# Optimization experiments

Hardware: AMD Instinct MI355X
Metric: run time of the kernel (lower is better)

The kernel has to match this reference:

```python
import jax, jax.numpy as jnp
import numpy as np

B, T, N, E = 8, 16, 2048, 32768
F_IN, C, EDGE_DIM = 32, 32, 1


def setup_inputs() -> dict:
    key = jax.random.key(0)
    ks = jax.random.split(key, 12)
    s = 1.0 / np.sqrt(C)
    x = jax.random.normal(ks[0], (B, T, N, F_IN), jnp.float32)
    edge_index = jax.random.randint(ks[1], (2, E), 0, N)
    edge_attr = jax.random.normal(ks[2], (E, EDGE_DIM), jnp.float32)
    Wl = jax.random.normal(ks[3], (F_IN, C), jnp.float32) * s
    bl = jnp.zeros((C,), jnp.float32)
    Wr = jax.random.normal(ks[4], (F_IN, C), jnp.float32) * s
    br = jnp.zeros((C,), jnp.float32)
    We = jax.random.normal(ks[5], (EDGE_DIM, C), jnp.float32) * s
    att = jax.random.normal(ks[6], (C,), jnp.float32) * s
    out_bias = jnp.zeros((C,), jnp.float32)
    w_ih = jax.random.normal(ks[7], (3 * C, C), jnp.float32) * s
    w_hh = jax.random.normal(ks[8], (3 * C, C), jnp.float32) * s
    b_ih = jnp.zeros((3 * C,), jnp.float32)
    b_hh = jnp.zeros((3 * C,), jnp.float32)
    return dict(x=x, edge_index=edge_index, edge_attr=edge_attr, Wl=Wl, bl=bl,
                Wr=Wr, br=br, We=We, att=att, out_bias=out_bias,
                w_ih=w_ih, w_hh=w_hh, b_ih=b_ih, b_hh=b_hh)


def _gatv2(x, edge_index, edge_attr, Wl, bl, Wr, br, We, att, out_bias):
    # x: [B,T,N,F]; GATv2Conv, heads=1, negative_slope=0.2, self loops w/ mean edge attr
    n = x.shape[2]
    src, dst = edge_index[0], edge_index[1]
    deg = jax.ops.segment_sum(jnp.ones((src.shape[0],), x.dtype), dst, num_segments=n)
    mean_attr = jax.ops.segment_sum(edge_attr, dst, num_segments=n) / jnp.maximum(deg, 1.0)[:, None]
    loop = jnp.arange(n)
    src_a = jnp.concatenate([src, loop])
    dst_a = jnp.concatenate([dst, loop])
    attr_a = jnp.concatenate([edge_attr, mean_attr], axis=0)
    xl = x @ Wl + bl  # [B,T,N,C]
    xr = x @ Wr + br
    e_emb = attr_a @ We  # [E2,C]
    xls = jnp.take(xl, src_a, axis=2)  # [B,T,E2,C]
    m = jax.nn.leaky_relu(xls + jnp.take(xr, dst_a, axis=2) + e_emb, 0.2)
    s = jnp.einsum('btec,c->ebt', m, att)  # [E2,B,T]
    smax = jax.ops.segment_max(s, dst_a, num_segments=n)
    es = jnp.exp(s - smax[dst_a])
    denom = jax.ops.segment_sum(es, dst_a, num_segments=n)
    alpha = es / denom[dst_a]  # segment softmax over incoming edges, [E2,B,T]
    msg = xls * alpha.transpose(1, 2, 0)[..., None]  # [B,T,E2,C]
    out = jax.ops.segment_sum(msg.transpose(2, 0, 1, 3), dst_a, num_segments=n)
    return out.transpose(1, 2, 0, 3) + out_bias  # [B,T,N,C]


def _gru(seq, w_ih, w_hh, b_ih, b_hh):
    # seq: [BN, T, C]; torch GRU gate order r,z,n
    c = seq.shape[-1]

    def step(h, xt):
        gi = xt @ w_ih.T + b_ih
        gh = h @ w_hh.T + b_hh
        ir, iz, inn = jnp.split(gi, 3, axis=-1)
        hr, hz, hn = jnp.split(gh, 3, axis=-1)
        r = jax.nn.sigmoid(ir + hr)
        z = jax.nn.sigmoid(iz + hz)
        nc = jnp.tanh(inn + r * hn)
        h = (1.0 - z) * nc + z * h
        return h, h

    h0 = jnp.zeros((seq.shape[0], c), seq.dtype)
    _, ys = jax.lax.scan(step, h0, seq.transpose(1, 0, 2))
    return ys.transpose(1, 0, 2)


def reference(x, edge_index, edge_attr, Wl, bl, Wr, br, We, att, out_bias, w_ih, w_hh, b_ih, b_hh):
    b, t, n, _ = x.shape
    h = _gatv2(x, edge_index, edge_attr, Wl, bl, Wr, br, We, att, out_bias)
    seq = h.transpose(0, 2, 1, 3).reshape(b * n, t, -1)
    y = _gru(seq, w_ih, w_hh, b_ih, b_hh)
    return y.reshape(b, n, t, -1).transpose(0, 2, 1, 3)
```

## Files before the change

kernel.cpp:

```cpp
#include <hip/hip_runtime.h>
#include <hip/hip_bf16.h>

#define N_NODES 2048
#define N_EDGES 32768
#define BT      128
#define TT      16
#define CH      32
#define E2      (N_EDGES + N_NODES)

static __device__ __forceinline__ unsigned pk2(float a, float b) {
    __hip_bfloat162 h2(__float2bfloat16(a), __float2bfloat16(b));
    return *reinterpret_cast<unsigned*>(&h2);
}

__global__ void deg_attr_kernel(const int* __restrict__ ei,
                                const float* __restrict__ ea,
                                int* __restrict__ deg, float* __restrict__ asum) {
    int e = blockIdx.x * 256 + threadIdx.x;
    if (e < N_EDGES) {
        int dst = ei[N_EDGES + e];
        atomicAdd(&deg[dst], 1);
        atomicAdd(&asum[dst], ea[e]);
    }
}

__global__ void scan_kernel(const int* __restrict__ deg, int* __restrict__ rowp) {
    int lane = threadIdx.x;
    int base = lane * 32;
    int loc[32];
    int s = 0;
    #pragma unroll
    for (int i = 0; i < 32; ++i) { loc[i] = s; s += deg[base + i] + 1; }
    int inc = s;
    #pragma unroll
    for (int d = 1; d < 64; d <<= 1) {
        int v = __shfl_up(inc, d, 64);
        if (lane >= d) inc += v;
    }
    int excl = inc - s;
    #pragma unroll
    for (int i = 0; i < 32; ++i) rowp[base + i] = excl + loc[i];
    if (lane == 63) rowp[N_NODES] = inc;
}

__global__ void scatter_kernel(const int* __restrict__ ei,
                               const float* __restrict__ ea,
                               const int* __restrict__ deg, const float* __restrict__ asum,
                               const int* __restrict__ rowp, int* __restrict__ fill,
                               int* __restrict__ col, float* __restrict__ attr_s) {
    int e = blockIdx.x * 256 + threadIdx.x;
    if (e >= E2) return;
    int src, dst; float a;
    if (e < N_EDGES) {
        src = ei[e]; dst = ei[N_EDGES + e]; a = ea[e];
    } else {
        int n = e - N_EDGES;
        src = n; dst = n;
        a = asum[n] / fmaxf((float)deg[n], 1.0f);
    }
    int pos = atomicAdd(&fill[dst], 1);
    col[rowp[dst] + pos]    = src;
    attr_s[rowp[dst] + pos] = a;
}

__global__ __launch_bounds__(256) void proj_kernel(
        const float* __restrict__ x,
        const float* __restrict__ Wl, const float* __restrict__ bl,
        unsigned* __restrict__ xlt) {
    __shared__ float xs[128 * 32];
    __shared__ float wl[1024];
    int n = blockIdx.x;
    int tid = threadIdx.x;
    for (int i = tid; i < 1024; i += 256) wl[i] = Wl[i];
    #pragma unroll
    for (int i = 0; i < 16; ++i) {
        int e = i * 256 + tid;
        int bt = e >> 5, f = e & 31;
        xs[e] = x[((long)bt * N_NODES + n) * 32 + f];
    }
    __syncthreads();
    int c2  = tid & 15;
    int btl = tid >> 4;
    int c0 = 2 * c2, c1 = c0 + 1;
    float b0 = bl[c0], b1 = bl[c1];
    for (int i = 0; i < 8; ++i) {
        int bt = i * 16 + btl;
        float a0 = 0.f, a1 = 0.f;
        #pragma unroll
        for (int f = 0; f < 32; ++f) {
            float xv = xs[bt * 32 + f];
            a0 = fmaf(xv, wl[f * 32 + c0], a0);
            a1 = fmaf(xv, wl[f * 32 + c1], a1);
        }
        xlt[((long)n * 16 + c2) * 128 + bt] = pk2(a0 + b0, a1 + b1);
    }
}

__global__ __launch_bounds__(256) void gat_kernel(
        const unsigned* __restrict__ xlt,
        const float* __restrict__ x,
        const int* __restrict__ rowp, const int* __restrict__ col,
        const float* __restrict__ attr_s,
        const float* __restrict__ Wr, const float* __restrict__ br,
        const float* __restrict__ We, const float* __restrict__ att,
        const float* __restrict__ ob,
        const float* __restrict__ wih, const float* __restrict__ bih,
        __hip_bfloat16* __restrict__ gi) {
    int tid = threadIdx.x;
    int wv = tid >> 6, lane = tid & 63;
    int task = blockIdx.x * 4 + wv;
    int n   = task >> 1;
    int bt  = ((task & 1) << 6) | lane;

    float xf[32];
    {
        const float* xp = x + ((long)bt * N_NODES + n) * 32;
        #pragma unroll
        for (int f4 = 0; f4 < 8; ++f4) {
            float4 a = *(const float4*)(xp + f4 * 4);
            xf[f4*4+0]=a.x; xf[f4*4+1]=a.y; xf[f4*4+2]=a.z; xf[f4*4+3]=a.w;
        }
    }
    float xrv[32];
    #pragma unroll
    for (int c = 0; c < 32; ++c) {
        float s = br[c];
        #pragma unroll
        for (int f = 0; f < 32; ++f) s = fmaf(xf[f], Wr[f * 32 + c], s);
        xrv[c] = s;
    }

    float accv[32];
    #pragma unroll
    for (int c = 0; c < 32; ++c) accv[c] = 0.f;

    int beg = rowp[n];
    int end = rowp[n + 1];
    float den = 0.f;
    const unsigned* xbase = xlt + bt;
    for (int j = beg; j < end; ++j) {
        int   src = col[j];
        float av  = attr_s[j];
        const unsigned* gp = xbase + (long)src * (16 * 128);
        float xlv[32];
        #pragma unroll
        for (int c2 = 0; c2 < 16; ++c2) {
            unsigned u = gp[c2 * 128];
            xlv[2*c2]   = __uint_as_float(u << 16);
            xlv[2*c2+1] = __uint_as_float(u & 0xffff0000u);
        }
        float p0 = 0.f, p1 = 0.f, p2 = 0.f, p3 = 0.f;
        #pragma unroll
        for (int k = 0; k < 8; ++k) {
            { int c = k;      float m = xlv[c] + fmaf(av, We[c], xrv[c]); p0 = fmaf(att[c], fmaxf(m, 0.2f * m), p0); }
            { int c = k + 8;  float m = xlv[c] + fmaf(av, We[c], xrv[c]); p1 = fmaf(att[c], fmaxf(m, 0.2f * m), p1); }
            { int c = k + 16; float m = xlv[c] + fmaf(av, We[c], xrv[c]); p2 = fmaf(att[c], fmaxf(m, 0.2f * m), p2); }
            { int c = k + 24; float m = xlv[c] + fmaf(av, We[c], xrv[c]); p3 = fmaf(att[c], fmaxf(m, 0.2f * m), p3); }
        }
        float p = fminf((p0 + p1) + (p2 + p3), 80.f);
        float w = __expf(p);
        den += w;
        #pragma unroll
        for (int c = 0; c < 32; ++c) accv[c] = fmaf(w, xlv[c], accv[c]);
    }
    float inv = 1.f / den;
    #pragma unroll
    for (int c = 0; c < 32; ++c) accv[c] = fmaf(accv[c], inv, ob[c]);

    __hip_bfloat16* gip = gi + ((long)bt * N_NODES + n) * 96;
    #pragma unroll
    for (int g8 = 0; g8 < 12; ++g8) {
        float s0 = bih[g8*8+0], s1 = bih[g8*8+1], s2 = bih[g8*8+2], s3 = bih[g8*8+3];
        float s4 = bih[g8*8+4], s5 = bih[g8*8+5], s6 = bih[g8*8+6], s7 = bih[g8*8+7];
        #pragma unroll
        for (int f = 0; f < 32; ++f) {
            float hf = accv[f];
            s0 = fmaf(hf, wih[(g8*8+0)*32+f], s0);
            s1 = fmaf(hf, wih[(g8*8+1)*32+f], s1);
            s2 = fmaf(hf, wih[(g8*8+2)*32+f], s2);
            s3 = fmaf(hf, wih[(g8*8+3)*32+f], s3);
            s4 = fmaf(hf, wih[(g8*8+4)*32+f], s4);
            s5 = fmaf(hf, wih[(g8*8+5)*32+f], s5);
            s6 = fmaf(hf, wih[(g8*8+6)*32+f], s6);
            s7 = fmaf(hf, wih[(g8*8+7)*32+f], s7);
        }
        uint4 v;
        v.x = pk2(s0, s1); v.y = pk2(s2, s3); v.z = pk2(s4, s5); v.w = pk2(s6, s7);
        *(uint4*)(gip + g8 * 8) = v;
    }
}

__global__ __launch_bounds__(256) void gru_kernel(
        const float* __restrict__ whh, const float* __restrict__ bhh,
        const __hip_bfloat16* __restrict__ gi,
        float* __restrict__ out) {
    int tid  = threadIdx.x;
    int lane = tid & 63;
    int c    = lane & 31;
    int half = lane >> 5;
    int fbase = half << 4;
    int seq  = blockIdx.x * 4 + (tid >> 6);
    int b = seq >> 11;
    int n = seq & 2047;

    float w0[16], w1[16], w2[16];
    #pragma unroll
    for (int k4 = 0; k4 < 4; ++k4) {
        float4 a0 = *(const float4*)&whh[( 0 + c) * 32 + fbase + k4 * 4];
        float4 a1 = *(const float4*)&whh[(32 + c) * 32 + fbase + k4 * 4];
        float4 a2 = *(const float4*)&whh[(64 + c) * 32 + fbase + k4 * 4];
        w0[k4*4+0]=a0.x; w0[k4*4+1]=a0.y; w0[k4*4+2]=a0.z; w0[k4*4+3]=a0.w;
        w1[k4*4+0]=a1.x; w1[k4*4+1]=a1.y; w1[k4*4+2]=a1.z; w1[k4*4+3]=a1.w;
        w2[k4*4+0]=a2.x; w2[k4*4+1]=a2.y; w2[k4*4+2]=a2.z; w2[k4*4+3]=a2.w;
    }
    float bh0 = half ? 0.f : bhh[c];
    float bh1 = half ? 0.f : bhh[32 + c];
    float bh2 = half ? 0.f : bhh[64 + c];

    const long GSTR = (long)N_NODES * 96;
    long gbase = ((long)b * TT * N_NODES + n) * 96 + c;
    const long OSTR = (long)N_NODES * CH;
    long obase = ((long)b * TT * N_NODES + n) * CH + c;

    float hc = 0.f;
    float gr = __bfloat162float(gi[gbase]);
    float gz = __bfloat162float(gi[gbase + 32]);
    float gn = __bfloat162float(gi[gbase + 64]);
    #pragma unroll 1
    for (int t = 0; t < TT; ++t) {
        long gnx = gbase + (long)(t + 1) * GSTR;
        float grn = 0.f, gzn = 0.f, gnn = 0.f;
        if (t + 1 < TT) {
            grn = __bfloat162float(gi[gnx]);
            gzn = __bfloat162float(gi[gnx + 32]);
            gnn = __bfloat162float(gi[gnx + 64]);
        }
        float g0 = bh0, g1 = bh1, g2 = bh2;
        #pragma unroll
        for (int k = 0; k < 16; ++k) {
            float v = __shfl(hc, fbase + k, 64);
            g0 = fmaf(v, w0[k], g0);
            g1 = fmaf(v, w1[k], g1);
            g2 = fmaf(v, w2[k], g2);
        }
        float G0 = g0 + __shfl_xor(g0, 32, 64);
        float G1 = g1 + __shfl_xor(g1, 32, 64);
        float G2 = g2 + __shfl_xor(g2, 32, 64);
        float r  = 1.f / (1.f + __expf(-(gr + G0)));
        float z  = 1.f / (1.f + __expf(-(gz + G1)));
        float a  = fmaf(r, G2, gn);
        float e2 = __expf(2.f * a);
        float nc = 1.f - 2.f / (e2 + 1.f);
        hc = (1.f - z) * nc + z * hc;
        if (half == 0) out[obase + (long)t * OSTR] = hc;
        gr = grn; gz = gzn; gn = gnn;
    }
}

extern "C" void kernel_launch(void* const* d_in, const int* in_sizes, int n_in,
                              void* d_out, int out_size, void* d_ws, size_t ws_size,
                              hipStream_t stream) {
    const float* x    = (const float*)d_in[0];
    const int*   ei   = (const int*)d_in[1];
    const float* ea   = (const float*)d_in[2];
    const float* Wl   = (const float*)d_in[3];
    const float* bl   = (const float*)d_in[4];
    const float* Wr   = (const float*)d_in[5];
    const float* br   = (const float*)d_in[6];
    const float* We   = (const float*)d_in[7];
    const float* att  = (const float*)d_in[8];
    const float* ob   = (const float*)d_in[9];
    const float* wih  = (const float*)d_in[10];
    const float* whh  = (const float*)d_in[11];
    const float* bih  = (const float*)d_in[12];
    const float* bhh  = (const float*)d_in[13];
    float* out = (float*)d_out;

    int*   deg  = (int*)d_ws;
    float* asum = (float*)(deg + N_NODES);
    int*   fill = (int*)(asum + N_NODES);
    int*   rowp = fill + N_NODES;
    int*   col  = rowp + (N_NODES + 16);
    float* attr_s = (float*)(col + E2);
    unsigned* xlt = (unsigned*)(attr_s + E2);
    xlt = (unsigned*)(((uintptr_t)xlt + 255) & ~(uintptr_t)255);
    __hip_bfloat16* gi = (__hip_bfloat16*)(xlt + (long)N_NODES * 16 * 128);

    hipMemsetAsync(deg, 0, 3 * N_NODES * sizeof(int), stream);

    deg_attr_kernel<<<N_EDGES / 256, 256, 0, stream>>>(ei, ea, deg, asum);
    scan_kernel<<<1, 64, 0, stream>>>(deg, rowp);
    scatter_kernel<<<(E2 + 255) / 256, 256, 0, stream>>>(ei, ea, deg, asum, rowp, fill, col, attr_s);
    proj_kernel<<<N_NODES, 256, 0, stream>>>(x, Wl, bl, xlt);
    gat_kernel<<<(N_NODES * 2) / 4, 256, 0, stream>>>(xlt, x, rowp, col, attr_s,
                                                      Wr, br, We, att, ob, wih, bih, gi);
    gru_kernel<<<(BT / TT * N_NODES) / 4, 256, 0, stream>>>(whh, bhh, gi, out);
}
```

Before: 233.6 us.

## Relayout xl for 128-bit gathers and split edges across wave halves

Changes the projected xl layout so each (node, bt) row of 16 packed bf16 pairs is contiguous, letting the GAT gather use four uint4 loads instead of sixteen strided scalar loads. Each wave now covers 32 bt values for one node, with the two half-waves handling alternate edges and combining partial sums through cross-half shuffles. The W_ih output projection is split between the two halves, and block indices are remapped so blocks landing on the same XCD share node and bt ranges, aiming for better L2 locality. In exchange the grid doubles and the x load plus Wr projection are computed twice per (node, bt), once in each half-wave.

```diff
diff --git a/kernel.cpp b/kernel.cpp
--- a/kernel.cpp
+++ b/kernel.cpp
@@ -92,7 +92,7 @@
             a0 = fmaf(xv, wl[f * 32 + c0], a0);
             a1 = fmaf(xv, wl[f * 32 + c1], a1);
         }
-        xlt[((long)n * 16 + c2) * 128 + bt] = pk2(a0 + b0, a1 + b1);
+        xlt[(long)n * 2048 + (bt >> 5) * 512 + (bt & 31) * 16 + c2] = pk2(a0 + b0, a1 + b1);
     }
 }
 
@@ -106,70 +106,90 @@
         const float* __restrict__ ob,
         const float* __restrict__ wih, const float* __restrict__ bih,
         __hip_bfloat16* __restrict__ gi) {
-    int tid = threadIdx.x;
-    int wv = tid >> 6, lane = tid & 63;
-    int task = blockIdx.x * 4 + wv;
-    int n   = task >> 1;
-    int bt  = ((task & 1) << 6) | lane;
-
-    float xf[32];
+    int tid  = threadIdx.x;
+    int wv   = tid >> 6;
+    int lane = tid & 63;
+    int epar = lane >> 5;
+    int btl  = lane & 31;
+    int bid  = blockIdx.x;
+    int xcd  = bid & 7;
+    int btq  = xcd >> 1;
+    int n    = ((xcd & 1) << 10) | ((bid >> 3) << 2) | wv;
+    int bt   = (btq << 5) | btl;
+
+    float xrv[32];
     {
+        float xf[32];
         const float* xp = x + ((long)bt * N_NODES + n) * 32;
         #pragma unroll
         for (int f4 = 0; f4 < 8; ++f4) {
             float4 a = *(const float4*)(xp + f4 * 4);
             xf[f4*4+0]=a.x; xf[f4*4+1]=a.y; xf[f4*4+2]=a.z; xf[f4*4+3]=a.w;
         }
-    }
-    float xrv[32];
-    #pragma unroll
-    for (int c = 0; c < 32; ++c) {
-        float s = br[c];
-        #pragma unroll
-        for (int f = 0; f < 32; ++f) s = fmaf(xf[f], Wr[f * 32 + c], s);
-        xrv[c] = s;
+        #pragma unroll
+        for (int c = 0; c < 32; ++c) {
+            float s = br[c];
+            #pragma unroll
+            for (int f = 0; f < 32; ++f) s = fmaf(xf[f], Wr[f * 32 + c], s);
+            xrv[c] = s;
+        }
     }
 
     float accv[32];
     #pragma unroll
     for (int c = 0; c < 32; ++c) accv[c] = 0.f;
+    float den = 0.f;
 
     int beg = rowp[n];
     int end = rowp[n + 1];
-    float den = 0.f;
-    const unsigned* xbase = xlt + bt;
-    for (int j = beg; j < end; ++j) {
+    const unsigned* xqbase = xlt + (long)btq * 512 + btl * 16;
+
+    for (int j = beg + epar; j < end; j += 2) {
         int   src = col[j];
         float av  = attr_s[j];
-        const unsigned* gp = xbase + (long)src * (16 * 128);
-        float xlv[32];
+        const uint4* gp = (const uint4*)(xqbase + (long)src * 2048);
+        uint4 A = gp[0], B = gp[1], C = gp[2], D = gp[3];
+        unsigned u[16];
+        u[0]=A.x; u[1]=A.y; u[2]=A.z;  u[3]=A.w;
+        u[4]=B.x; u[5]=B.y; u[6]=B.z;  u[7]=B.w;
+        u[8]=C.x; u[9]=C.y; u[10]=C.z; u[11]=C.w;
+        u[12]=D.x; u[13]=D.y; u[14]=D.z; u[15]=D.w;
+
+        float p0 = 0.f, p1 = 0.f, p2 = 0.f, p3 = 0.f;
         #pragma unroll
         for (int c2 = 0; c2 < 16; ++c2) {
-            unsigned u = gp[c2 * 128];
-            xlv[2*c2]   = __uint_as_float(u << 16);
-            xlv[2*c2+1] = __uint_as_float(u & 0xffff0000u);
-        }
-        float p0 = 0.f, p1 = 0.f, p2 = 0.f, p3 = 0.f;
-        #pragma unroll
-        for (int k = 0; k < 8; ++k) {
-            { int c = k;      float m = xlv[c] + fmaf(av, We[c], xrv[c]); p0 = fmaf(att[c], fmaxf(m, 0.2f * m), p0); }
-            { int c = k + 8;  float m = xlv[c] + fmaf(av, We[c], xrv[c]); p1 = fmaf(att[c], fmaxf(m, 0.2f * m), p1); }
-            { int c = k + 16; float m = xlv[c] + fmaf(av, We[c], xrv[c]); p2 = fmaf(att[c], fmaxf(m, 0.2f * m), p2); }
-            { int c = k + 24; float m = xlv[c] + fmaf(av, We[c], xrv[c]); p3 = fmaf(att[c], fmaxf(m, 0.2f * m), p3); }
+            unsigned w2 = u[c2];
+            float x0 = __uint_as_float(w2 << 16);
+            float x1 = __uint_as_float(w2 & 0xffff0000u);
+            int c = 2 * c2;
+            float m0 = x0 + fmaf(av, We[c],     xrv[c]);
+            float m1 = x1 + fmaf(av, We[c + 1], xrv[c + 1]);
+            if (c2 & 1) { p2 = fmaf(att[c], fmaxf(m0, 0.2f * m0), p2);
+                          p3 = fmaf(att[c + 1], fmaxf(m1, 0.2f * m1), p3); }
+            else        { p0 = fmaf(att[c], fmaxf(m0, 0.2f * m0), p0);
+                          p1 = fmaf(att[c + 1], fmaxf(m1, 0.2f * m1), p1); }
         }
         float p = fminf((p0 + p1) + (p2 + p3), 80.f);
         float w = __expf(p);
         den += w;
         #pragma unroll
-        for (int c = 0; c < 32; ++c) accv[c] = fmaf(w, xlv[c], accv[c]);
-    }
+        for (int c2 = 0; c2 < 16; ++c2) {
+            unsigned w2 = u[c2];
+            accv[2*c2]   = fmaf(w, __uint_as_float(w2 << 16),         accv[2*c2]);
+            accv[2*c2+1] = fmaf(w, __uint_as_float(w2 & 0xffff0000u), accv[2*c2+1]);
+        }
+    }
+    den += __shfl_xor(den, 32, 64);
+    #pragma unroll
+    for (int c = 0; c < 32; ++c) accv[c] += __shfl_xor(accv[c], 32, 64);
+
     float inv = 1.f / den;
     #pragma unroll
     for (int c = 0; c < 32; ++c) accv[c] = fmaf(accv[c], inv, ob[c]);
 
     __hip_bfloat16* gip = gi + ((long)bt * N_NODES + n) * 96;
-    #pragma unroll
-    for (int g8 = 0; g8 < 12; ++g8) {
+    int g8lo = epar * 6, g8hi = g8lo + 6;
+    for (int g8 = g8lo; g8 < g8hi; ++g8) {
         float s0 = bih[g8*8+0], s1 = bih[g8*8+1], s2 = bih[g8*8+2], s3 = bih[g8*8+3];
         float s4 = bih[g8*8+4], s5 = bih[g8*8+5], s6 = bih[g8*8+6], s7 = bih[g8*8+7];
         #pragma unroll
@@ -284,7 +304,7 @@
     float* attr_s = (float*)(col + E2);
     unsigned* xlt = (unsigned*)(attr_s + E2);
     xlt = (unsigned*)(((uintptr_t)xlt + 255) & ~(uintptr_t)255);
-    __hip_bfloat16* gi = (__hip_bfloat16*)(xlt + (long)N_NODES * 16 * 128);
+    __hip_bfloat16* gi = (__hip_bfloat16*)(xlt + (long)N_NODES * 2048);
 
     hipMemsetAsync(deg, 0, 3 * N_NODES * sizeof(int), stream);
 
@@ -292,7 +312,7 @@
     scan_kernel<<<1, 64, 0, stream>>>(deg, rowp);
     scatter_kernel<<<(E2 + 255) / 256, 256, 0, stream>>>(ei, ea, deg, asum, rowp, fill, col, attr_s);
     proj_kernel<<<N_NODES, 256, 0, stream>>>(x, Wl, bl, xlt);
-    gat_kernel<<<(N_NODES * 2) / 4, 256, 0, stream>>>(xlt, x, rowp, col, attr_s,
-                                                      Wr, br, We, att, ob, wih, bih, gi);
+    gat_kernel<<<2048, 256, 0, stream>>>(xlt, x, rowp, col, attr_s,
+                                         Wr, br, We, att, ob, wih, bih, gi);
     gru_kernel<<<(BT / TT * N_NODES) / 4, 256, 0, stream>>>(whh, bhh, gi, out);
 }
```

New measurement: 267.6 us. 1.15x slower.
